# Kernel tuning notes

Hardware: AMD Instinct MI355X
Metric: run time of the kernel (lower is better)

## Reference

```python
import jax, jax.numpy as jnp
import numpy as np

N, L, H, D_HEAD, P = 2, 1024, 8, 64, 1
DIM = H * D_HEAD


def setup_inputs() -> dict:
    key0 = jax.random.key(0)
    ks = jax.random.split(key0, 7)
    query = jax.random.normal(ks[0], (N, L, DIM), dtype=jnp.float32)
    key = jax.random.normal(ks[1], (N, L, DIM), dtype=jnp.float32)
    scale = 1.0 / np.sqrt(DIM)
    Wq = jax.random.normal(ks[2], (DIM, DIM), dtype=jnp.float32) * scale
    Wk = jax.random.normal(ks[3], (DIM, DIM), dtype=jnp.float32) * scale
    Wv = jax.random.normal(ks[4], (DIM, DIM), dtype=jnp.float32) * scale
    position_weight = jax.random.uniform(ks[5], (H, P, D_HEAD), dtype=jnp.float32) * 2 - 1
    position_bias = jax.random.uniform(ks[6], (H, D_HEAD), dtype=jnp.float32) * 2 - 1
    return {"query": query, "key": key, "Wq": Wq, "Wk": Wk, "Wv": Wv,
            "position_weight": position_weight, "position_bias": position_bias}


def _kernel_fn(x):
    # _log_exp_kernel: positive feature map log(1 + exp(x)) (softplus)
    return jax.nn.softplus(x)


def _causal_term(qf, kf, v):
    """Linear-complexity causal attention term.
    qf, kf: (N,H,L,d) feature-mapped query/key; v: (N,H,L,d) values.
    Returns numerator (N,H,L,d) and denominator (N,H,L)."""
    # cumulative key-value outer products: (N,H,L,d,d)
    kv = jnp.cumsum(jnp.einsum('nhkd,nhke->nhkde', kf, v), axis=2)
    num = jnp.einsum('nhqd,nhqde->nhqe', qf, kv)
    den = jnp.einsum('nhqd,nhqd->nhq', qf, jnp.cumsum(kf, axis=2))
    return num, den


def reference(query, key, Wq, Wk, Wv, position_weight, position_bias):
    n, lq, dim = query.shape
    lk = key.shape[1]
    h, p, d = position_weight.shape
    kernel = _kernel_fn
    # projections (torch Linear: x @ W.T), reshape to heads, transpose to (N,H,L,d)
    q = kernel((query @ Wq.T).reshape(n, lq, h, d)).transpose(0, 2, 1, 3)
    k = kernel((key @ Wk.T).reshape(n, lk, h, d)).transpose(0, 2, 1, 3)
    v = ((key @ Wv.T).reshape(n, lk, h, d)).transpose(0, 2, 1, 3)
    # default positions: arange, expanded to (N,L,P)
    qpos = jnp.broadcast_to(jnp.arange(lq, dtype=query.dtype)[None, :, None], (n, lq, p))
    kpos = jnp.broadcast_to(jnp.arange(lk, dtype=key.dtype)[None, :, None], (n, lk, p))
    pq = jnp.einsum('nlp,hpd->nhld', qpos, position_weight) \
         + jax.nn.sigmoid(position_bias)[None, :, None, :] * jnp.pi
    pk = jnp.einsum('nlp,hpd->nhld', kpos, position_weight)
    # three branches: cos, sin, plain (trig identity split of cos(pq - pk) RPE)
    num_c, den_c = _causal_term(q * jnp.cos(pq), k * jnp.cos(pk), v)
    num_s, den_s = _causal_term(q * jnp.sin(pq), k * jnp.sin(pk), v)
    num_p, den_p = _causal_term(q, k, v)
    num = num_c + num_s + num_p
    den = den_c + den_s + den_p
    attention = num / den[..., None]  # scaled=True
    return attention.transpose(0, 2, 1, 3).reshape(n, lq, dim)
```

## Files before the change

### kernel.cpp

```cpp
#include <hip/hip_runtime.h>
#include <hip/hip_bf16.h>

#define LSEQ   1024
#define NHEAD  8
#define DH     64
#define DIM    512
#define CHUNK  64
#define NCHUNK 16
#define NHTOT  16
#define LDB    68
#define LDA    72

typedef __attribute__((ext_vector_type(8))) short short8;
typedef __attribute__((ext_vector_type(4))) float floatx4;

__device__ __forceinline__ float softplusf_(float x) {
    if (x > 20.f) return x;
    return log1pf(expf(x));
}
__device__ __forceinline__ unsigned short bf16_rne(float x) {
    unsigned int u = __float_as_uint(x);
    u += 0x7FFFu + ((u >> 16) & 1u);
    return (unsigned short)(u >> 16);
}
__device__ __forceinline__ float bf16_tof(unsigned short h) {
    return __uint_as_float(((unsigned int)h) << 16);
}

__global__ __launch_bounds__(256) void proj_kernel(
    const float* __restrict__ query, const float* __restrict__ key,
    const float* __restrict__ Wq, const float* __restrict__ Wk,
    const float* __restrict__ Wv,
    unsigned short* __restrict__ qbuf, unsigned short* __restrict__ kbuf,
    unsigned short* __restrict__ vbuf)
{
    const int mt  = blockIdx.x;
    const int ot  = blockIdx.y;
    const int sel = blockIdx.z;
    const int t   = threadIdx.x;

    const float* __restrict__ X = (sel == 0) ? query : key;
    const float* __restrict__ W = (sel == 0) ? Wq : (sel == 1) ? Wk : Wv;
    unsigned short* __restrict__ obuf = (sel == 0) ? qbuf : (sel == 1) ? kbuf : vbuf;

    __shared__ unsigned short As[64 * LDB];
    __shared__ unsigned short Bs[64 * LDB];

    const int m0 = mt * 64, o0 = ot * 64;
    const int lane = t & 63, wave = t >> 6;
    const int quad = lane >> 4, l16 = lane & 15;
    const int wm = wave >> 1, wn = wave & 1;

    const int srow = t >> 2;
    const int sc16 = (t & 3) * 16;

    floatx4 acc[2][2];
    #pragma unroll
    for (int i = 0; i < 2; ++i)
        #pragma unroll
        for (int j = 0; j < 2; ++j) acc[i][j] = (floatx4){0.f, 0.f, 0.f, 0.f};

    float4 ax[4], bx4[4];
    #pragma unroll
    for (int i = 0; i < 4; ++i) {
        ax[i]  = *(const float4*)&X[(size_t)(m0 + srow) * DIM + sc16 + i * 4];
        bx4[i] = *(const float4*)&W[(size_t)(o0 + srow) * DIM + sc16 + i * 4];
    }

    for (int kt = 0; kt < DIM; kt += 64) {
        __syncthreads();
        {
            short8 a0, a1, b0, b1;
            #pragma unroll
            for (int i = 0; i < 2; ++i) {
                const float va[4] = {ax[i].x, ax[i].y, ax[i].z, ax[i].w};
                const float vb[4] = {bx4[i].x, bx4[i].y, bx4[i].z, bx4[i].w};
                #pragma unroll
                for (int j = 0; j < 4; ++j) {
                    a0[i * 4 + j] = (short)bf16_rne(va[j]);
                    b0[i * 4 + j] = (short)bf16_rne(vb[j]);
                }
            }
            #pragma unroll
            for (int i = 2; i < 4; ++i) {
                const float va[4] = {ax[i].x, ax[i].y, ax[i].z, ax[i].w};
                const float vb[4] = {bx4[i].x, bx4[i].y, bx4[i].z, bx4[i].w};
                #pragma unroll
                for (int j = 0; j < 4; ++j) {
                    a1[(i - 2) * 4 + j] = (short)bf16_rne(va[j]);
                    b1[(i - 2) * 4 + j] = (short)bf16_rne(vb[j]);
                }
            }
            *(short8*)&As[srow * LDB + sc16]     = a0;
            *(short8*)&As[srow * LDB + sc16 + 8] = a1;
            *(short8*)&Bs[srow * LDB + sc16]     = b0;
            *(short8*)&Bs[srow * LDB + sc16 + 8] = b1;
        }
        __syncthreads();

        if (kt + 64 < DIM) {
            #pragma unroll
            for (int i = 0; i < 4; ++i) {
                ax[i]  = *(const float4*)&X[(size_t)(m0 + srow) * DIM + kt + 64 + sc16 + i * 4];
                bx4[i] = *(const float4*)&W[(size_t)(o0 + srow) * DIM + kt + 64 + sc16 + i * 4];
            }
        }

        #pragma unroll
        for (int s = 0; s < 2; ++s) {
            short8 af[2], bf[2];
            #pragma unroll
            for (int mi = 0; mi < 2; ++mi)
                af[mi] = *(const short8*)&As[(wm * 32 + mi * 16 + l16) * LDB + s * 32 + quad * 8];
            #pragma unroll
            for (int ni = 0; ni < 2; ++ni)
                bf[ni] = *(const short8*)&Bs[(wn * 32 + ni * 16 + l16) * LDB + s * 32 + quad * 8];
            #pragma unroll
            for (int ni = 0; ni < 2; ++ni)
                #pragma unroll
                for (int mi = 0; mi < 2; ++mi)
                    acc[mi][ni] = __builtin_amdgcn_mfma_f32_16x16x32_bf16(af[mi], bf[ni], acc[mi][ni], 0, 0, 0);
        }
    }

    const int h = ot;
    #pragma unroll
    for (int mi = 0; mi < 2; ++mi)
        #pragma unroll
        for (int ni = 0; ni < 2; ++ni) {
            const int d = wn * 32 + ni * 16 + l16;
            #pragma unroll
            for (int r = 0; r < 4; ++r) {
                const int m = m0 + wm * 32 + mi * 16 + quad * 4 + r;
                const int n = m >> 10, l = m & (LSEQ - 1);
                float val = acc[mi][ni][r];
                if (sel < 2) val = softplusf_(val);
                obuf[(((size_t)(n * NHEAD + h)) * LSEQ + l) * DH + d] = bf16_rne(val);
            }
        }
}

__global__ __launch_bounds__(256) void chunksum_kernel(
    const unsigned short* __restrict__ kbuf, const unsigned short* __restrict__ vbuf,
    const float* __restrict__ pw,
    float* __restrict__ Ssum, float* __restrict__ zsum)
{
    const int c  = blockIdx.x;
    const int nh = blockIdx.y;
    const int br = blockIdx.z;
    const int h  = nh & (NHEAD - 1);
    const int t  = threadIdx.x;
    const int lane = t & 63, wave = t >> 6;
    const int quad = lane >> 4, l16 = lane & 15;
    const int wm = wave >> 1, wn = wave & 1;

    __shared__ unsigned short kfT[64 * LDA];
    __shared__ unsigned short vT[64 * LDA];
    __shared__ float dpart[4][64];

    const size_t base = ((size_t)nh * LSEQ + (size_t)c * CHUNK) * DH;

    {
        const int col = t & 63;
        const int kq  = (t >> 6) * 16;
        const float w = pw[h * DH + col];
        unsigned short kfv[16], vvv[16];
        #pragma unroll
        for (int j = 0; j < 16; ++j) {
            const int k = kq + j;
            const unsigned short kraw = kbuf[base + (size_t)k * DH + col];
            vvv[j] = vbuf[base + (size_t)k * DH + col];
            if (br == 0) kfv[j] = kraw;
            else {
                const float pos = (float)(c * CHUNK + k);
                const float f = (br == 1) ? cosf(pos * w) : sinf(pos * w);
                kfv[j] = bf16_rne(bf16_tof(kraw) * f);
            }
        }
        #pragma unroll
        for (int g = 0; g < 4; ++g) {
            ushort4 a, b;
            a.x = kfv[g * 4]; a.y = kfv[g * 4 + 1]; a.z = kfv[g * 4 + 2]; a.w = kfv[g * 4 + 3];
            b.x = vvv[g * 4]; b.y = vvv[g * 4 + 1]; b.z = vvv[g * 4 + 2]; b.w = vvv[g * 4 + 3];
            *(ushort4*)&kfT[col * LDA + kq + g * 4] = a;
            *(ushort4*)&vT[col * LDA + kq + g * 4]  = b;
        }
    }
    __syncthreads();

    floatx4 acc[2][2];
    #pragma unroll
    for (int i = 0; i < 2; ++i)
        #pragma unroll
        for (int j = 0; j < 2; ++j) acc[i][j] = (floatx4){0.f, 0.f, 0.f, 0.f};

    #pragma unroll
    for (int kk = 0; kk < 2; ++kk) {
        short8 a[2], b[2];
        #pragma unroll
        for (int mi = 0; mi < 2; ++mi)
            a[mi] = *(const short8*)&vT[(wm * 32 + mi * 16 + l16) * LDA + kk * 32 + quad * 8];
        #pragma unroll
        for (int ni = 0; ni < 2; ++ni)
            b[ni] = *(const short8*)&kfT[(wn * 32 + ni * 16 + l16) * LDA + kk * 32 + quad * 8];
        #pragma unroll
        for (int ni = 0; ni < 2; ++ni)
            #pragma unroll
            for (int mi = 0; mi < 2; ++mi)
                acc[mi][ni] = __builtin_amdgcn_mfma_f32_16x16x32_bf16(a[mi], b[ni], acc[mi][ni], 0, 0, 0);
    }

    {
        const int d = t & 63, seg = t >> 6;
        float s = 0.f;
        #pragma unroll
        for (int j2 = 0; j2 < 2; ++j2) {
            const short8 v8 = *(const short8*)&kfT[d * LDA + seg * 16 + j2 * 8];
            #pragma unroll
            for (int j = 0; j < 8; ++j) s += bf16_tof((unsigned short)v8[j]);
        }
        dpart[seg][d] = s;
    }
    __syncthreads();
    if (t < DH) {
        zsum[((size_t)(br * NHTOT + nh) * NCHUNK + c) * DH + t] =
            dpart[0][t] + dpart[1][t] + dpart[2][t] + dpart[3][t];
    }

    float* Sg = Ssum + ((size_t)(br * NHTOT + nh) * NCHUNK + c) * (DH * DH);
    #pragma unroll
    for (int mi = 0; mi < 2; ++mi)
        #pragma unroll
        for (int ni = 0; ni < 2; ++ni) {
            const int d = wn * 32 + ni * 16 + l16;
            #pragma unroll
            for (int r = 0; r < 4; ++r) {
                const int e = wm * 32 + mi * 16 + quad * 4 + r;
                Sg[e * DH + d] = acc[mi][ni][r];
            }
        }
}

__global__ __launch_bounds__(256) void scan_kernel(
    float* __restrict__ Ssum, float* __restrict__ zsum)
{
    const int b = blockIdx.x;
    const int s = blockIdx.y;
    const int idx = s * 256 + threadIdx.x;

    float* S = Ssum + (size_t)b * NCHUNK * (DH * DH);
    float v[NCHUNK];
    #pragma unroll
    for (int c = 0; c < NCHUNK; ++c) v[c] = S[c * (DH * DH) + idx];
    float run = 0.f;
    #pragma unroll
    for (int c = 0; c < NCHUNK; ++c) {
        const float nv = v[c];
        S[c * (DH * DH) + idx] = run;
        run += nv;
    }
    if (s == 0 && threadIdx.x < DH) {
        float* z = zsum + (size_t)b * NCHUNK * DH;
        float zv[NCHUNK];
        #pragma unroll
        for (int c = 0; c < NCHUNK; ++c) zv[c] = z[c * DH + threadIdx.x];
        float zr = 0.f;
        #pragma unroll
        for (int c = 0; c < NCHUNK; ++c) {
            const float nv = zv[c];
            z[c * DH + threadIdx.x] = zr;
            zr += nv;
        }
    }
}

__global__ __launch_bounds__(256) void attn_kernel(
    const unsigned short* __restrict__ qbuf, const unsigned short* __restrict__ kbuf,
    const unsigned short* __restrict__ vbuf,
    const float* __restrict__ Ssum, const float* __restrict__ zsum,
    const float* __restrict__ pw, const float* __restrict__ pb,
    unsigned short* __restrict__ numP, float* __restrict__ denP)
{
    const int c  = blockIdx.x;
    const int nh = blockIdx.y;
    const int br = blockIdx.z;
    const int n  = nh >> 3;
    const int h  = nh & (NHEAD - 1);
    const int t  = threadIdx.x;
    const int lane = t & 63, wave = t >> 6;
    const int quad = lane >> 4, l16 = lane & 15;
    const int wm = wave >> 1, wn = wave & 1;

    __shared__ unsigned short qfL[64 * LDA];
    __shared__ unsigned short kfL[64 * LDA];
    __shared__ unsigned short vTL[64 * LDA];
    __shared__ unsigned short SpL[64 * LDA];
    __shared__ unsigned short scA[64 * LDA];
    __shared__ float zl[DH];
    __shared__ float dpart[8][64];

    const size_t base = ((size_t)nh * LSEQ + (size_t)c * CHUNK) * DH;
    const float* Sg = Ssum + ((size_t)(br * NHTOT + nh) * NCHUNK + c) * (DH * DH);
    const float PI_ = 3.14159265358979323846f;

    {
        const int col = t & 63;
        const int kq  = (t >> 6) * 16;
        unsigned short vvv[16];
        #pragma unroll
        for (int j = 0; j < 16; ++j)
            vvv[j] = vbuf[base + (size_t)(kq + j) * DH + col];
        #pragma unroll
        for (int g = 0; g < 4; ++g) {
            ushort4 b;
            b.x = vvv[g * 4]; b.y = vvv[g * 4 + 1]; b.z = vvv[g * 4 + 2]; b.w = vvv[g * 4 + 3];
            *(ushort4*)&vTL[col * LDA + kq + g * 4] = b;
        }
    }

    #pragma unroll
    for (int i = 0; i < 4; ++i) {
        const int idx = i * 256 + t;
        const int r  = idx >> 4;
        const int c4 = (idx & 15) * 4;
        const ushort4 qv = *(const ushort4*)&qbuf[base + (size_t)r * DH + c4];
        const ushort4 kv = *(const ushort4*)&kbuf[base + (size_t)r * DH + c4];
        const float4  sv = *(const float4*)&Sg[r * DH + c4];
        const unsigned short* pq0 = (const unsigned short*)&qv;
        const unsigned short* pk0 = (const unsigned short*)&kv;
        ushort4 qh, kh, sh;
        unsigned short* pq = (unsigned short*)&qh;
        unsigned short* pk = (unsigned short*)&kh;
        unsigned short* ps = (unsigned short*)&sh;
        if (br == 0) {
            #pragma unroll
            for (int j = 0; j < 4; ++j) { pq[j] = pq0[j]; pk[j] = pk0[j]; }
        } else {
            const float4 wv  = *(const float4*)&pw[h * DH + c4];
            const float4 pbv = *(const float4*)&pb[h * DH + c4];
            const float w4[4] = {wv.x, wv.y, wv.z, wv.w};
            const float b4[4] = {pbv.x, pbv.y, pbv.z, pbv.w};
            const float pos = (float)(c * CHUNK + r);
            #pragma unroll
            for (int j = 0; j < 4; ++j) {
                const float bias = PI_ / (1.f + expf(-b4[j]));
                float tq, tk;
                if (br == 1) { tq = cosf(pos * w4[j] + bias); tk = cosf(pos * w4[j]); }
                else         { tq = sinf(pos * w4[j] + bias); tk = sinf(pos * w4[j]); }
                pq[j] = bf16_rne(bf16_tof(pq0[j]) * tq);
                pk[j] = bf16_rne(bf16_tof(pk0[j]) * tk);
            }
        }
        const float s4[4] = {sv.x, sv.y, sv.z, sv.w};
        #pragma unroll
        for (int j = 0; j < 4; ++j) ps[j] = bf16_rne(s4[j]);
        *(ushort4*)&qfL[r * LDA + c4] = qh;
        *(ushort4*)&kfL[r * LDA + c4] = kh;
        *(ushort4*)&SpL[r * LDA + c4] = sh;
    }
    if (t < DH)
        zl[t] = zsum[((size_t)(br * NHTOT + nh) * NCHUNK + c) * DH + t];
    __syncthreads();

    floatx4 acc1[2][2], acc2[2][2];
    #pragma unroll
    for (int i = 0; i < 2; ++i)
        #pragma unroll
        for (int j = 0; j < 2; ++j) {
            acc1[i][j] = (floatx4){0.f, 0.f, 0.f, 0.f};
            acc2[i][j] = (floatx4){0.f, 0.f, 0.f, 0.f};
        }
    #pragma unroll
    for (int kk = 0; kk < 2; ++kk) {
        short8 a[2], b1[2], b2[2];
        #pragma unroll
        for (int mi = 0; mi < 2; ++mi)
            a[mi] = *(const short8*)&qfL[(wm * 32 + mi * 16 + l16) * LDA + kk * 32 + quad * 8];
        #pragma unroll
        for (int ni = 0; ni < 2; ++ni) {
            b1[ni] = *(const short8*)&kfL[(wn * 32 + ni * 16 + l16) * LDA + kk * 32 + quad * 8];
            b2[ni] = *(const short8*)&SpL[(wn * 32 + ni * 16 + l16) * LDA + kk * 32 + quad * 8];
        }
        #pragma unroll
        for (int ni = 0; ni < 2; ++ni)
            #pragma unroll
            for (int mi = 0; mi < 2; ++mi) {
                acc1[mi][ni] = __builtin_amdgcn_mfma_f32_16x16x32_bf16(a[mi], b1[ni], acc1[mi][ni], 0, 0, 0);
                acc2[mi][ni] = __builtin_amdgcn_mfma_f32_16x16x32_bf16(a[mi], b2[ni], acc2[mi][ni], 0, 0, 0);
            }
    }

    {
        const int l = t & 63, seg = t >> 6;
        float s = 0.f;
        #pragma unroll
        for (int j2 = 0; j2 < 2; ++j2) {
            const short8 v8 = *(const short8*)&qfL[l * LDA + seg * 16 + j2 * 8];
            #pragma unroll
            for (int j = 0; j < 8; ++j)
                s += bf16_tof((unsigned short)v8[j]) * zl[seg * 16 + j2 * 8 + j];
        }
        dpart[seg][l] = s;
    }

    #pragma unroll
    for (int mi = 0; mi < 2; ++mi)
        #pragma unroll
        for (int ni = 0; ni < 2; ++ni) {
            const int kcol = wn * 32 + ni * 16 + l16;
            #pragma unroll
            for (int r = 0; r < 4; ++r) {
                const int lrow = wm * 32 + mi * 16 + quad * 4 + r;
                const float v = (kcol <= lrow) ? acc1[mi][ni][r] : 0.f;
                scA[lrow * LDA + kcol] = bf16_rne(v);
            }
        }
    __syncthreads();

    #pragma unroll
    for (int kk = 0; kk < 2; ++kk) {
        short8 a[2], b[2];
        #pragma unroll
        for (int mi = 0; mi < 2; ++mi)
            a[mi] = *(const short8*)&scA[(wm * 32 + mi * 16 + l16) * LDA + kk * 32 + quad * 8];
        #pragma unroll
        for (int ni = 0; ni < 2; ++ni)
            b[ni] = *(const short8*)&vTL[(wn * 32 + ni * 16 + l16) * LDA + kk * 32 + quad * 8];
        #pragma unroll
        for (int ni = 0; ni < 2; ++ni)
            #pragma unroll
            for (int mi = 0; mi < 2; ++mi)
                acc2[mi][ni] = __builtin_amdgcn_mfma_f32_16x16x32_bf16(a[mi], b[ni], acc2[mi][ni], 0, 0, 0);
    }

    {
        const int l = t & 63, seg = t >> 6;
        float s = 0.f;
        #pragma unroll
        for (int j2 = 0; j2 < 2; ++j2) {
            const short8 v8 = *(const short8*)&scA[l * LDA + seg * 16 + j2 * 8];
            #pragma unroll
            for (int j = 0; j < 8; ++j) s += bf16_tof((unsigned short)v8[j]);
        }
        dpart[4 + seg][l] = s;
    }
    __syncthreads();

    if (t < DH) {
        const float dl = dpart[0][t] + dpart[1][t] + dpart[2][t] + dpart[3][t]
                       + dpart[4][t] + dpart[5][t] + dpart[6][t] + dpart[7][t];
        denP[((size_t)(br * NHTOT + nh)) * LSEQ + c * CHUNK + t] = dl;
    }

    #pragma unroll
    for (int mi = 0; mi < 2; ++mi)
        #pragma unroll
        for (int ni = 0; ni < 2; ++ni) {
            const int e = wn * 32 + ni * 16 + l16;
            #pragma unroll
            for (int r = 0; r < 4; ++r) {
                const int l = c * CHUNK + wm * 32 + mi * 16 + quad * 4 + r;
                numP[(((size_t)br * 2 + n) * LSEQ + l) * DIM + h * DH + e] =
                    bf16_rne(acc2[mi][ni][r]);
            }
        }
}

__global__ __launch_bounds__(256) void combine_kernel(
    const unsigned short* __restrict__ numP, const float* __restrict__ denP,
    float* __restrict__ outp)
{
    const int i = blockIdx.x * 256 + threadIdx.x;
    const int row = i >> 7;
    const int ci  = i & 127;
    const int n = row >> 10, l = row & (LSEQ - 1), h = ci >> 4;
    const int nh = n * NHEAD + h;
    const ushort4* N = (const ushort4*)numP;
    const ushort4 a = N[i];
    const ushort4 b = N[i + 262144];
    const ushort4 cc = N[i + 524288];
    const float ds = denP[(size_t)nh * LSEQ + l]
                   + denP[((size_t)NHTOT + nh) * LSEQ + l]
                   + denP[((size_t)2 * NHTOT + nh) * LSEQ + l];
    const float inv = 1.f / ds;
    float4 o;
    o.x = (bf16_tof(a.x) + bf16_tof(b.x) + bf16_tof(cc.x)) * inv;
    o.y = (bf16_tof(a.y) + bf16_tof(b.y) + bf16_tof(cc.y)) * inv;
    o.z = (bf16_tof(a.z) + bf16_tof(b.z) + bf16_tof(cc.z)) * inv;
    o.w = (bf16_tof(a.w) + bf16_tof(b.w) + bf16_tof(cc.w)) * inv;
    ((float4*)outp)[i] = o;
}

extern "C" void kernel_launch(void* const* d_in, const int* in_sizes, int n_in,
                              void* d_out, int out_size, void* d_ws, size_t ws_size,
                              hipStream_t stream) {
    const float* query = (const float*)d_in[0];
    const float* key   = (const float*)d_in[1];
    const float* Wq    = (const float*)d_in[2];
    const float* Wk    = (const float*)d_in[3];
    const float* Wv    = (const float*)d_in[4];
    const float* pw    = (const float*)d_in[5];
    const float* pb    = (const float*)d_in[6];

    unsigned short* U = (unsigned short*)d_ws;
    float* F = (float*)d_ws;
    unsigned short* qbuf = U;
    unsigned short* kbuf = U + 1048576;
    unsigned short* vbuf = U + 2097152;
    float* Ssum = F + 1572864;
    float* zsum = F + 4718592;
    unsigned short* numP = U + 9535488;
    float* denP = F + 6340608;

    proj_kernel<<<dim3(32, 8, 3), 256, 0, stream>>>(
        query, key, Wq, Wk, Wv, qbuf, kbuf, vbuf);
    chunksum_kernel<<<dim3(NCHUNK, NHTOT, 3), 256, 0, stream>>>(
        kbuf, vbuf, pw, Ssum, zsum);
    scan_kernel<<<dim3(3 * NHTOT, NCHUNK), 256, 0, stream>>>(Ssum, zsum);
    attn_kernel<<<dim3(NCHUNK, NHTOT, 3), 256, 0, stream>>>(
        qbuf, kbuf, vbuf, Ssum, zsum, pw, pb, numP, denP);
    combine_kernel<<<dim3(1024), 256, 0, stream>>>(numP, denP, (float*)d_out);
}
```

Measured before the change: 124.6 us.

## Fuse branch sum and normalization into attn kernel, split query rows per block

```diff
diff --git a/kernel.cpp b/kernel.cpp
--- a/kernel.cpp
+++ b/kernel.cpp
@@ -279,11 +279,11 @@
     const unsigned short* __restrict__ vbuf,
     const float* __restrict__ Ssum, const float* __restrict__ zsum,
     const float* __restrict__ pw, const float* __restrict__ pb,
-    unsigned short* __restrict__ numP, float* __restrict__ denP)
+    float* __restrict__ outp)
 {
     const int c  = blockIdx.x;
     const int nh = blockIdx.y;
-    const int br = blockIdx.z;
+    const int lh = blockIdx.z;
     const int n  = nh >> 3;
     const int h  = nh & (NHEAD - 1);
     const int t  = threadIdx.x;
@@ -291,16 +291,16 @@
     const int quad = lane >> 4, l16 = lane & 15;
     const int wm = wave >> 1, wn = wave & 1;
 
-    __shared__ unsigned short qfL[64 * LDA];
+    __shared__ unsigned short vTL[64 * LDA];
     __shared__ unsigned short kfL[64 * LDA];
-    __shared__ unsigned short vTL[64 * LDA];
     __shared__ unsigned short SpL[64 * LDA];
-    __shared__ unsigned short scA[64 * LDA];
+    __shared__ unsigned short qfL[32 * LDA];
+    __shared__ unsigned short scA[32 * LDA];
     __shared__ float zl[DH];
-    __shared__ float dpart[8][64];
+    __shared__ float dpart[8][32];
+    __shared__ float dl[32];
 
     const size_t base = ((size_t)nh * LSEQ + (size_t)c * CHUNK) * DH;
-    const float* Sg = Ssum + ((size_t)(br * NHTOT + nh) * NCHUNK + c) * (DH * DH);
     const float PI_ = 3.14159265358979323846f;
 
     {
@@ -318,177 +318,159 @@
         }
     }
 
-    #pragma unroll
-    for (int i = 0; i < 4; ++i) {
-        const int idx = i * 256 + t;
-        const int r  = idx >> 4;
-        const int c4 = (idx & 15) * 4;
-        const ushort4 qv = *(const ushort4*)&qbuf[base + (size_t)r * DH + c4];
-        const ushort4 kv = *(const ushort4*)&kbuf[base + (size_t)r * DH + c4];
-        const float4  sv = *(const float4*)&Sg[r * DH + c4];
-        const unsigned short* pq0 = (const unsigned short*)&qv;
-        const unsigned short* pk0 = (const unsigned short*)&kv;
-        ushort4 qh, kh, sh;
-        unsigned short* pq = (unsigned short*)&qh;
-        unsigned short* pk = (unsigned short*)&kh;
-        unsigned short* ps = (unsigned short*)&sh;
-        if (br == 0) {
-            #pragma unroll
-            for (int j = 0; j < 4; ++j) { pq[j] = pq0[j]; pk[j] = pk0[j]; }
-        } else {
-            const float4 wv  = *(const float4*)&pw[h * DH + c4];
-            const float4 pbv = *(const float4*)&pb[h * DH + c4];
-            const float w4[4] = {wv.x, wv.y, wv.z, wv.w};
-            const float b4[4] = {pbv.x, pbv.y, pbv.z, pbv.w};
-            const float pos = (float)(c * CHUNK + r);
-            #pragma unroll
-            for (int j = 0; j < 4; ++j) {
-                const float bias = PI_ / (1.f + expf(-b4[j]));
-                float tq, tk;
-                if (br == 1) { tq = cosf(pos * w4[j] + bias); tk = cosf(pos * w4[j]); }
-                else         { tq = sinf(pos * w4[j] + bias); tk = sinf(pos * w4[j]); }
-                pq[j] = bf16_rne(bf16_tof(pq0[j]) * tq);
-                pk[j] = bf16_rne(bf16_tof(pk0[j]) * tk);
-            }
-        }
-        const float s4[4] = {sv.x, sv.y, sv.z, sv.w};
-        #pragma unroll
-        for (int j = 0; j < 4; ++j) ps[j] = bf16_rne(s4[j]);
-        *(ushort4*)&qfL[r * LDA + c4] = qh;
-        *(ushort4*)&kfL[r * LDA + c4] = kh;
-        *(ushort4*)&SpL[r * LDA + c4] = sh;
-    }
-    if (t < DH)
-        zl[t] = zsum[((size_t)(br * NHTOT + nh) * NCHUNK + c) * DH + t];
+    floatx4 accS[2], accN[2];
+    #pragma unroll
+    for (int i = 0; i < 2; ++i) {
+        accS[i] = (floatx4){0.f, 0.f, 0.f, 0.f};
+        accN[i] = (floatx4){0.f, 0.f, 0.f, 0.f};
+    }
+    float den_reg = 0.f;
+
+    for (int br = 0; br < 3; ++br) {
+        __syncthreads();
+
+        const float* Sg = Ssum + ((size_t)(br * NHTOT + nh) * NCHUNK + c) * (DH * DH);
+        #pragma unroll
+        for (int i = 0; i < 4; ++i) {
+            const int idx = i * 256 + t;
+            const int r  = idx >> 4;
+            const int c4 = (idx & 15) * 4;
+            const ushort4 kv = *(const ushort4*)&kbuf[base + (size_t)r * DH + c4];
+            const float4  sv = *(const float4*)&Sg[r * DH + c4];
+            const unsigned short* pk0 = (const unsigned short*)&kv;
+            ushort4 kh, sh;
+            unsigned short* pk = (unsigned short*)&kh;
+            unsigned short* ps = (unsigned short*)&sh;
+            if (br == 0) {
+                #pragma unroll
+                for (int j = 0; j < 4; ++j) pk[j] = pk0[j];
+            } else {
+                const float4 wv = *(const float4*)&pw[h * DH + c4];
+                const float w4[4] = {wv.x, wv.y, wv.z, wv.w};
+                const float pos = (float)(c * CHUNK + r);
+                #pragma unroll
+                for (int j = 0; j < 4; ++j) {
+                    const float tk = (br == 1) ? cosf(pos * w4[j]) : sinf(pos * w4[j]);
+                    pk[j] = bf16_rne(bf16_tof(pk0[j]) * tk);
+                }
+            }
+            const float s4[4] = {sv.x, sv.y, sv.z, sv.w};
+            #pragma unroll
+            for (int j = 0; j < 4; ++j) ps[j] = bf16_rne(s4[j]);
+            *(ushort4*)&kfL[r * LDA + c4] = kh;
+            *(ushort4*)&SpL[r * LDA + c4] = sh;
+        }
+
+        #pragma unroll
+        for (int i = 0; i < 2; ++i) {
+            const int idx = i * 256 + t;
+            const int r  = idx >> 4;
+            const int c4 = (idx & 15) * 4;
+            const int rg = lh * 32 + r;
+            const ushort4 qv = *(const ushort4*)&qbuf[base + (size_t)rg * DH + c4];
+            const unsigned short* pq0 = (const unsigned short*)&qv;
+            ushort4 qh;
+            unsigned short* pq = (unsigned short*)&qh;
+            if (br == 0) {
+                #pragma unroll
+                for (int j = 0; j < 4; ++j) pq[j] = pq0[j];
+            } else {
+                const float4 wv  = *(const float4*)&pw[h * DH + c4];
+                const float4 pbv = *(const float4*)&pb[h * DH + c4];
+                const float w4[4] = {wv.x, wv.y, wv.z, wv.w};
+                const float b4[4] = {pbv.x, pbv.y, pbv.z, pbv.w};
+                const float pos = (float)(c * CHUNK + rg);
+                #pragma unroll
+                for (int j = 0; j < 4; ++j) {
+                    const float bias = PI_ / (1.f + expf(-b4[j]));
+                    const float tq = (br == 1) ? cosf(pos * w4[j] + bias)
+                                               : sinf(pos * w4[j] + bias);
+                    pq[j] = bf16_rne(bf16_tof(pq0[j]) * tq);
+                }
+            }
+            *(ushort4*)&qfL[r * LDA + c4] = qh;
+        }
+        if (t < DH)
+            zl[t] = zsum[((size_t)(br * NHTOT + nh) * NCHUNK + c) * DH + t];
+        __syncthreads();
+
+        #pragma unroll
+        for (int kk = 0; kk < 2; ++kk) {
+            const short8 a = *(const short8*)&qfL[(wm * 16 + l16) * LDA + kk * 32 + quad * 8];
+            short8 b1[2], b2[2];
+            #pragma unroll
+            for (int ni = 0; ni < 2; ++ni) {
+                b1[ni] = *(const short8*)&kfL[(wn * 32 + ni * 16 + l16) * LDA + kk * 32 + quad * 8];
+                b2[ni] = *(const short8*)&SpL[(wn * 32 + ni * 16 + l16) * LDA + kk * 32 + quad * 8];
+            }
+            #pragma unroll
+            for (int ni = 0; ni < 2; ++ni) {
+                accS[ni] = __builtin_amdgcn_mfma_f32_16x16x32_bf16(a, b1[ni], accS[ni], 0, 0, 0);
+                accN[ni] = __builtin_amdgcn_mfma_f32_16x16x32_bf16(a, b2[ni], accN[ni], 0, 0, 0);
+            }
+        }
+
+        {
+            const int l = t & 31, dseg = t >> 5;
+            float s = 0.f;
+            #pragma unroll
+            for (int j = 0; j < 8; ++j) {
+                const int d = dseg * 8 + j;
+                s += bf16_tof(qfL[l * LDA + d]) * zl[d];
+            }
+            den_reg += s;
+        }
+    }
+
+    #pragma unroll
+    for (int ni = 0; ni < 2; ++ni) {
+        const int kcol = wn * 32 + ni * 16 + l16;
+        #pragma unroll
+        for (int r = 0; r < 4; ++r) {
+            const int lrow = wm * 16 + quad * 4 + r;
+            const float v = (kcol <= lh * 32 + lrow) ? accS[ni][r] : 0.f;
+            scA[lrow * LDA + kcol] = bf16_rne(v);
+        }
+    }
     __syncthreads();
 
-    floatx4 acc1[2][2], acc2[2][2];
-    #pragma unroll
-    for (int i = 0; i < 2; ++i)
-        #pragma unroll
-        for (int j = 0; j < 2; ++j) {
-            acc1[i][j] = (floatx4){0.f, 0.f, 0.f, 0.f};
-            acc2[i][j] = (floatx4){0.f, 0.f, 0.f, 0.f};
-        }
     #pragma unroll
     for (int kk = 0; kk < 2; ++kk) {
-        short8 a[2], b1[2], b2[2];
-        #pragma unroll
-        for (int mi = 0; mi < 2; ++mi)
-            a[mi] = *(const short8*)&qfL[(wm * 32 + mi * 16 + l16) * LDA + kk * 32 + quad * 8];
+        const short8 a = *(const short8*)&scA[(wm * 16 + l16) * LDA + kk * 32 + quad * 8];
         #pragma unroll
         for (int ni = 0; ni < 2; ++ni) {
-            b1[ni] = *(const short8*)&kfL[(wn * 32 + ni * 16 + l16) * LDA + kk * 32 + quad * 8];
-            b2[ni] = *(const short8*)&SpL[(wn * 32 + ni * 16 + l16) * LDA + kk * 32 + quad * 8];
-        }
-        #pragma unroll
-        for (int ni = 0; ni < 2; ++ni)
-            #pragma unroll
-            for (int mi = 0; mi < 2; ++mi) {
-                acc1[mi][ni] = __builtin_amdgcn_mfma_f32_16x16x32_bf16(a[mi], b1[ni], acc1[mi][ni], 0, 0, 0);
-                acc2[mi][ni] = __builtin_amdgcn_mfma_f32_16x16x32_bf16(a[mi], b2[ni], acc2[mi][ni], 0, 0, 0);
-            }
+            const short8 b = *(const short8*)&vTL[(wn * 32 + ni * 16 + l16) * LDA + kk * 32 + quad * 8];
+            accN[ni] = __builtin_amdgcn_mfma_f32_16x16x32_bf16(a, b, accN[ni], 0, 0, 0);
+        }
     }
 
     {
-        const int l = t & 63, seg = t >> 6;
+        const int l = t & 31, kseg = t >> 5;
         float s = 0.f;
         #pragma unroll
-        for (int j2 = 0; j2 < 2; ++j2) {
-            const short8 v8 = *(const short8*)&qfL[l * LDA + seg * 16 + j2 * 8];
-            #pragma unroll
-            for (int j = 0; j < 8; ++j)
-                s += bf16_tof((unsigned short)v8[j]) * zl[seg * 16 + j2 * 8 + j];
-        }
-        dpart[seg][l] = s;
-    }
-
-    #pragma unroll
-    for (int mi = 0; mi < 2; ++mi)
-        #pragma unroll
-        for (int ni = 0; ni < 2; ++ni) {
-            const int kcol = wn * 32 + ni * 16 + l16;
-            #pragma unroll
-            for (int r = 0; r < 4; ++r) {
-                const int lrow = wm * 32 + mi * 16 + quad * 4 + r;
-                const float v = (kcol <= lrow) ? acc1[mi][ni][r] : 0.f;
-                scA[lrow * LDA + kcol] = bf16_rne(v);
-            }
-        }
+        for (int j = 0; j < 8; ++j)
+            s += bf16_tof(scA[l * LDA + kseg * 8 + j]);
+        dpart[kseg][l] = den_reg + s;
+    }
     __syncthreads();
-
-    #pragma unroll
-    for (int kk = 0; kk < 2; ++kk) {
-        short8 a[2], b[2];
-        #pragma unroll
-        for (int mi = 0; mi < 2; ++mi)
-            a[mi] = *(const short8*)&scA[(wm * 32 + mi * 16 + l16) * LDA + kk * 32 + quad * 8];
-        #pragma unroll
-        for (int ni = 0; ni < 2; ++ni)
-            b[ni] = *(const short8*)&vTL[(wn * 32 + ni * 16 + l16) * LDA + kk * 32 + quad * 8];
-        #pragma unroll
-        for (int ni = 0; ni < 2; ++ni)
-            #pragma unroll
-            for (int mi = 0; mi < 2; ++mi)
-                acc2[mi][ni] = __builtin_amdgcn_mfma_f32_16x16x32_bf16(a[mi], b[ni], acc2[mi][ni], 0, 0, 0);
-    }
-
-    {
-        const int l = t & 63, seg = t >> 6;
+    if (t < 32) {
         float s = 0.f;
         #pragma unroll
-        for (int j2 = 0; j2 < 2; ++j2) {
-            const short8 v8 = *(const short8*)&scA[l * LDA + seg * 16 + j2 * 8];
-            #pragma unroll
-            for (int j = 0; j < 8; ++j) s += bf16_tof((unsigned short)v8[j]);
-        }
-        dpart[4 + seg][l] = s;
+        for (int g = 0; g < 8; ++g) s += dpart[g][t];
+        dl[t] = 1.f / s;
     }
     __syncthreads();
 
-    if (t < DH) {
-        const float dl = dpart[0][t] + dpart[1][t] + dpart[2][t] + dpart[3][t]
-                       + dpart[4][t] + dpart[5][t] + dpart[6][t] + dpart[7][t];
-        denP[((size_t)(br * NHTOT + nh)) * LSEQ + c * CHUNK + t] = dl;
-    }
-
-    #pragma unroll
-    for (int mi = 0; mi < 2; ++mi)
-        #pragma unroll
-        for (int ni = 0; ni < 2; ++ni) {
-            const int e = wn * 32 + ni * 16 + l16;
-            #pragma unroll
-            for (int r = 0; r < 4; ++r) {
-                const int l = c * CHUNK + wm * 32 + mi * 16 + quad * 4 + r;
-                numP[(((size_t)br * 2 + n) * LSEQ + l) * DIM + h * DH + e] =
-                    bf16_rne(acc2[mi][ni][r]);
-            }
-        }
-}
-
-__global__ __launch_bounds__(256) void combine_kernel(
-    const unsigned short* __restrict__ numP, const float* __restrict__ denP,
-    float* __restrict__ outp)
-{
-    const int i = blockIdx.x * 256 + threadIdx.x;
-    const int row = i >> 7;
-    const int ci  = i & 127;
-    const int n = row >> 10, l = row & (LSEQ - 1), h = ci >> 4;
-    const int nh = n * NHEAD + h;
-    const ushort4* N = (const ushort4*)numP;
-    const ushort4 a = N[i];
-    const ushort4 b = N[i + 262144];
-    const ushort4 cc = N[i + 524288];
-    const float ds = denP[(size_t)nh * LSEQ + l]
-                   + denP[((size_t)NHTOT + nh) * LSEQ + l]
-                   + denP[((size_t)2 * NHTOT + nh) * LSEQ + l];
-    const float inv = 1.f / ds;
-    float4 o;
-    o.x = (bf16_tof(a.x) + bf16_tof(b.x) + bf16_tof(cc.x)) * inv;
-    o.y = (bf16_tof(a.y) + bf16_tof(b.y) + bf16_tof(cc.y)) * inv;
-    o.z = (bf16_tof(a.z) + bf16_tof(b.z) + bf16_tof(cc.z)) * inv;
-    o.w = (bf16_tof(a.w) + bf16_tof(b.w) + bf16_tof(cc.w)) * inv;
-    ((float4*)outp)[i] = o;
+    #pragma unroll
+    for (int ni = 0; ni < 2; ++ni) {
+        const int e = wn * 32 + ni * 16 + l16;
+        #pragma unroll
+        for (int r = 0; r < 4; ++r) {
+            const int lrow = wm * 16 + quad * 4 + r;
+            const int l = c * CHUNK + lh * 32 + lrow;
+            outp[((size_t)n * LSEQ + l) * DIM + h * DH + e] = accN[ni][r] * dl[lrow];
+        }
+    }
 }
 
 extern "C" void kernel_launch(void* const* d_in, const int* in_sizes, int n_in,
@@ -509,15 +491,12 @@
     unsigned short* vbuf = U + 2097152;
     float* Ssum = F + 1572864;
     float* zsum = F + 4718592;
-    unsigned short* numP = U + 9535488;
-    float* denP = F + 6340608;
 
     proj_kernel<<<dim3(32, 8, 3), 256, 0, stream>>>(
         query, key, Wq, Wk, Wv, qbuf, kbuf, vbuf);
     chunksum_kernel<<<dim3(NCHUNK, NHTOT, 3), 256, 0, stream>>>(
         kbuf, vbuf, pw, Ssum, zsum);
     scan_kernel<<<dim3(3 * NHTOT, NCHUNK), 256, 0, stream>>>(Ssum, zsum);
-    attn_kernel<<<dim3(NCHUNK, NHTOT, 3), 256, 0, stream>>>(
-        qbuf, kbuf, vbuf, Ssum, zsum, pw, pb, numP, denP);
-    combine_kernel<<<dim3(1024), 256, 0, stream>>>(numP, denP, (float*)d_out);
-}
+    attn_kernel<<<dim3(NCHUNK, NHTOT, 2), 256, 0, stream>>>(
+        qbuf, kbuf, vbuf, Ssum, zsum, pw, pb, (float*)d_out);
+}
```

New measurement: 124.3 us. About the same (-0.2%).
